# Optimization experiments

Measured on AMD Instinct MI355X. Metric: run time of the kernel, lower is better.

## Reference

```python
import jax, jax.numpy as jnp
import numpy as np

N_NODES = 100000


def gcn_conv(x, W, b, src, dst, norm, n_nodes):
    # x: [N, F_in] -> [N, F_out]; GCNConv: D^-1/2 (A+I) D^-1/2 (X W) + b
    h = x @ W                                   # [N, F_out]
    msg = h[src] * norm[:, None]                # [E+N, F_out] gather + scale
    out = jax.ops.segment_sum(msg, dst, num_segments=n_nodes)  # scatter-add
    return out + b


def setup_inputs() -> dict:
    key = jax.random.key(0)
    k0, k1, k2, k3, k4, k5 = jax.random.split(key, 6)
    n, e, f_in, f_hid, n_cls = N_NODES, 1600000, 128, 128, 3
    x = jax.random.normal(k0, (n, f_in), dtype=jnp.float32)
    edge_index = jax.random.randint(k1, (2, e), 0, n, dtype=jnp.int64)
    s1 = 1.0 / np.sqrt(f_in)
    s2 = 1.0 / np.sqrt(f_hid)
    W1 = jax.random.uniform(k2, (f_in, f_hid), jnp.float32, -s1, s1)
    b1 = jnp.zeros((f_hid,), jnp.float32)
    W2 = jax.random.uniform(k3, (f_hid, f_hid), jnp.float32, -s2, s2)
    b2 = jnp.zeros((f_hid,), jnp.float32)
    Wfc = jax.random.uniform(k4, (f_hid, n_cls), jnp.float32, -s2, s2)
    bfc = jax.random.uniform(k5, (n_cls,), jnp.float32, -s2, s2)
    return {"x": x, "edge_index": edge_index, "W1": W1, "b1": b1,
            "W2": W2, "b2": b2, "Wfc": Wfc, "bfc": bfc}


def reference(x, edge_index, W1, b1, W2, b2, Wfc, bfc):
    n = x.shape[0]
    # add self-loops (PyG GCNConv default add_self_loops=True)
    loops = jnp.arange(n, dtype=edge_index.dtype)
    src = jnp.concatenate([edge_index[0], loops])
    dst = jnp.concatenate([edge_index[1], loops])
    deg = jax.ops.segment_sum(jnp.ones_like(dst, dtype=x.dtype), dst,
                              num_segments=n)
    dinv = jax.lax.rsqrt(deg)                   # deg >= 1 due to self-loops
    norm = dinv[src] * dinv[dst]                # [E+N]
    h = jax.nn.relu(gcn_conv(x, W1, b1, src, dst, norm, n))   # dropout=eval id
    h = jax.nn.relu(gcn_conv(h, W2, b2, src, dst, norm, n))
    return jnp.tanh(h @ Wfc + bfc)              # [N, 3]
```

## Files before the change

kernel.cpp:

```cpp
#include <hip/hip_runtime.h>
#include <hip/hip_bf16.h>
#include <hip/hip_fp16.h>


#define NODE_F 128

typedef __attribute__((ext_vector_type(8))) short bf16x8;
typedef __attribute__((ext_vector_type(4))) float f32x4;

__device__ inline unsigned short bf16_rn(float x) {
    unsigned u = __builtin_bit_cast(unsigned, x);
    unsigned r = (u + 0x7fffu + ((u >> 16) & 1u)) >> 16;
    return (unsigned short)r;
}
__device__ inline float bf16_to_f(unsigned short h) {
    unsigned u = (unsigned)h << 16;
    return __builtin_bit_cast(float, u);
}


__global__ void deg_rank_kernel(const int* __restrict__ dst, int* __restrict__ degE,
                                int* __restrict__ rank, int E) {
    int i = blockIdx.x * blockDim.x + threadIdx.x;
    if (i < E) rank[i] = atomicAdd(&degE[dst[i]], 1);
}

__global__ __launch_bounds__(256) void scan_block_kernel(
    const int* __restrict__ degE, int* __restrict__ row_start,
    int* __restrict__ bsum, int N)
{
    __shared__ int s[256];
    const int tid = threadIdx.x;
    const int idx = blockIdx.x * 1024 + tid * 4;
    int v0 = (idx + 0 < N) ? degE[idx + 0] : 0;
    int v1 = (idx + 1 < N) ? degE[idx + 1] : 0;
    int v2 = (idx + 2 < N) ? degE[idx + 2] : 0;
    int v3 = (idx + 3 < N) ? degE[idx + 3] : 0;
    int t = v0 + v1 + v2 + v3;
    s[tid] = t;
    __syncthreads();
    #pragma unroll
    for (int off = 1; off < 256; off <<= 1) {
        int x = (tid >= off) ? s[tid - off] : 0;
        __syncthreads();
        s[tid] += x;
        __syncthreads();
    }
    int excl = s[tid] - t;
    if (idx + 0 < N) row_start[idx + 0] = excl;
    if (idx + 1 < N) row_start[idx + 1] = excl + v0;
    if (idx + 2 < N) row_start[idx + 2] = excl + v0 + v1;
    if (idx + 3 < N) row_start[idx + 3] = excl + v0 + v1 + v2;
    if (tid == 255) bsum[blockIdx.x] = s[255];
}

__global__ __launch_bounds__(1024) void scan_tops_kernel(int* __restrict__ bsum, int nb) {
    __shared__ int s[1024];
    const int tid = threadIdx.x;
    int v = (tid < nb) ? bsum[tid] : 0;
    s[tid] = v;
    __syncthreads();
    #pragma unroll
    for (int off = 1; off < 1024; off <<= 1) {
        int x = (tid >= off) ? s[tid - off] : 0;
        __syncthreads();
        s[tid] += x;
        __syncthreads();
    }
    if (tid < nb) bsum[tid] = s[tid] - v;
}

__global__ void scan_finish_kernel(const int* __restrict__ degE, int* __restrict__ row_start,
                                   const int* __restrict__ bsum, float* __restrict__ dinv, int N)
{
    int i = blockIdx.x * blockDim.x + threadIdx.x;
    if (i >= N) return;
    int rs = row_start[i] + bsum[i >> 10];
    row_start[i] = rs;
    dinv[i] = rsqrtf((float)degE[i] + 1.0f);
    if (i == N - 1) row_start[N] = rs + degE[i];
}


__global__ __launch_bounds__(256) void wconv_kernel(const float* __restrict__ W1,
                                                    const float* __restrict__ W2,
                                                    unsigned short* __restrict__ WhiT,
                                                    unsigned short* __restrict__ WloT)
{
    const float* W = blockIdx.x ? W2 : W1;
    unsigned short* hiT = WhiT + blockIdx.x * 128 * 128;
    unsigned short* loT = WloT + blockIdx.x * 128 * 128;
    int tid = threadIdx.x;
    for (int i = tid; i < 128 * 128; i += 256) {
        int k = i >> 7, n = i & 127;
        float x = W[i];
        unsigned short hi = bf16_rn(x);
        float lo = x - bf16_to_f(hi);
        hiT[n * 128 + k] = hi;
        loT[n * 128 + k] = bf16_rn(lo);
    }
}


template<bool RELU_IN>
__device__ __forceinline__ void gemm_body(
    const float* __restrict__ X, const unsigned short* __restrict__ WhiT,
    const unsigned short* __restrict__ WloT, const float* __restrict__ dinv,
    __half* __restrict__ Hs, int N, int bid,
    unsigned short* xhi, unsigned short* xlo)
{
    const int tid  = threadIdx.x;
    const int lane = tid & 63;
    const int w    = tid >> 6;
    const int rbase = bid * 64;

    bf16x8 bhi[2][4], blo[2][4];
    {
        int n0   = w * 32 + (lane & 15);
        int koct = (lane >> 4) * 8;
        #pragma unroll
        for (int nt = 0; nt < 2; ++nt) {
            #pragma unroll
            for (int kk = 0; kk < 4; ++kk) {
                size_t o = (size_t)(n0 + nt * 16) * 128 + kk * 32 + koct;
                bhi[nt][kk] = *reinterpret_cast<const bf16x8*>(WhiT + o);
                blo[nt][kk] = *reinterpret_cast<const bf16x8*>(WloT + o);
            }
        }
    }

    #pragma unroll
    for (int it = 0; it < 8; ++it) {
        int f   = it * 256 + tid;
        int row = f >> 5;
        int k4  = f & 31;
        float4 v = make_float4(0.f, 0.f, 0.f, 0.f);
        if (rbase + row < N)
            v = *reinterpret_cast<const float4*>(X + (size_t)(rbase + row) * NODE_F + k4 * 4);
        if (RELU_IN) {
            v.x = fmaxf(v.x, 0.f); v.y = fmaxf(v.y, 0.f);
            v.z = fmaxf(v.z, 0.f); v.w = fmaxf(v.w, 0.f);
        }
        float xs[4] = {v.x, v.y, v.z, v.w};
        ushort4 h4, l4;
        unsigned short* hp = &h4.x;
        unsigned short* lp = &l4.x;
        #pragma unroll
        for (int j = 0; j < 4; ++j) {
            unsigned short hi = bf16_rn(xs[j]);
            hp[j] = hi;
            lp[j] = bf16_rn(xs[j] - bf16_to_f(hi));
        }
        int byte = row * 256 + ((k4 * 8) ^ ((row & 7) << 4));
        *reinterpret_cast<ushort4*>(reinterpret_cast<char*>(xhi) + byte) = h4;
        *reinterpret_cast<ushort4*>(reinterpret_cast<char*>(xlo) + byte) = l4;
    }
    __syncthreads();

    f32x4 acc[4][2];
    #pragma unroll
    for (int m = 0; m < 4; ++m)
        #pragma unroll
        for (int nt = 0; nt < 2; ++nt)
            acc[m][nt] = (f32x4){0.f, 0.f, 0.f, 0.f};

    #pragma unroll
    for (int kk = 0; kk < 4; ++kk) {
        #pragma unroll
        for (int m = 0; m < 4; ++m) {
            int row  = m * 16 + (lane & 15);
            int koff = kk * 64 + (lane >> 4) * 16;
            int byte = row * 256 + (koff ^ ((row & 7) << 4));
            bf16x8 ahi = *reinterpret_cast<const bf16x8*>(reinterpret_cast<char*>(xhi) + byte);
            bf16x8 alo = *reinterpret_cast<const bf16x8*>(reinterpret_cast<char*>(xlo) + byte);
            #pragma unroll
            for (int nt = 0; nt < 2; ++nt) {
                acc[m][nt] = __builtin_amdgcn_mfma_f32_16x16x32_bf16(ahi, bhi[nt][kk], acc[m][nt], 0, 0, 0);
                acc[m][nt] = __builtin_amdgcn_mfma_f32_16x16x32_bf16(ahi, blo[nt][kk], acc[m][nt], 0, 0, 0);
                acc[m][nt] = __builtin_amdgcn_mfma_f32_16x16x32_bf16(alo, bhi[nt][kk], acc[m][nt], 0, 0, 0);
            }
        }
    }

    #pragma unroll
    for (int m = 0; m < 4; ++m) {
        int row = rbase + m * 16 + (lane >> 4) * 4;
        int col = w * 32 + (lane & 15);
        #pragma unroll
        for (int nt = 0; nt < 2; ++nt) {
            #pragma unroll
            for (int r = 0; r < 4; ++r) {
                if (row + r < N)
                    Hs[(size_t)(row + r) * NODE_F + col + nt * 16] =
                        __float2half(acc[m][nt][r] * dinv[row + r]);
            }
        }
    }
}

__global__ __launch_bounds__(256) void gemm1_fill_kernel(
    const float* __restrict__ X, const unsigned short* __restrict__ WhiT,
    const unsigned short* __restrict__ WloT, const float* __restrict__ dinv,
    __half* __restrict__ Hs, int N, int gemm_blocks,
    const int* __restrict__ src, const int* __restrict__ dst,
    const int* __restrict__ rank, const int* __restrict__ row_start,
    int* __restrict__ csr_src, int E)
{
    __shared__ unsigned short xhi[64 * 128];
    __shared__ unsigned short xlo[64 * 128];
    if (blockIdx.x < (unsigned)gemm_blocks) {
        gemm_body<false>(X, WhiT, WloT, dinv, Hs, N, blockIdx.x, xhi, xlo);
    } else {
        int e = (blockIdx.x - gemm_blocks) * 256 + threadIdx.x;
        if (e < E)
            csr_src[row_start[dst[e]] + rank[e]] = src[e];
    }
}

template<bool RELU_IN>
__global__ __launch_bounds__(256) void gemm_mfma_kernel(
    const float* __restrict__ X, const unsigned short* __restrict__ WhiT,
    const unsigned short* __restrict__ WloT, const float* __restrict__ dinv,
    __half* __restrict__ Hs, int N)
{
    __shared__ unsigned short xhi[64 * 128];
    __shared__ unsigned short xlo[64 * 128];
    gemm_body<RELU_IN>(X, WhiT, WloT, dinv, Hs, N, blockIdx.x, xhi, xlo);
}

__global__ __launch_bounds__(256) void gather_kernel(
    const __half* __restrict__ Hs, const int* __restrict__ csr_src,
    const int* __restrict__ row_start, const float* __restrict__ dinv,
    const float* __restrict__ b, float* __restrict__ acc, int N)
{
    int node = (blockIdx.x * blockDim.x + threadIdx.x) >> 6;
    int lane = threadIdx.x & 63;
    if (node >= N) return;

    const __half2* H2 = reinterpret_cast<const __half2*>(Hs);
    float2 a = __half22float2(H2[(size_t)node * 64 + lane]);

    int i   = row_start[node];
    int end = row_start[node + 1];
    for (; i + 3 < end; i += 4) {
        int s0 = csr_src[i], s1 = csr_src[i + 1], s2 = csr_src[i + 2], s3 = csr_src[i + 3];
        float2 v0 = __half22float2(H2[(size_t)s0 * 64 + lane]);
        float2 v1 = __half22float2(H2[(size_t)s1 * 64 + lane]);
        float2 v2 = __half22float2(H2[(size_t)s2 * 64 + lane]);
        float2 v3 = __half22float2(H2[(size_t)s3 * 64 + lane]);
        a.x += (v0.x + v1.x) + (v2.x + v3.x);
        a.y += (v0.y + v1.y) + (v2.y + v3.y);
    }
    for (; i < end; ++i) {
        int s = csr_src[i];
        float2 v = __half22float2(H2[(size_t)s * 64 + lane]);
        a.x += v.x;
        a.y += v.y;
    }

    const float dd = dinv[node];
    float2 bb = reinterpret_cast<const float2*>(b)[lane];
    float2 o;
    o.x = bb.x + dd * a.x;
    o.y = bb.y + dd * a.y;
    reinterpret_cast<float2*>(acc)[(size_t)node * 64 + lane] = o;
}


__global__ __launch_bounds__(256) void fc_kernel(const float* __restrict__ A,
                                                 const float* __restrict__ Wfc,
                                                 const float* __restrict__ bfc,
                                                 float* __restrict__ out, int N)
{
    int wid  = (blockIdx.x * blockDim.x + threadIdx.x) >> 6;
    int lane = threadIdx.x & 63;
    if (wid >= N) return;
    const float* row = A + (size_t)wid * NODE_F;
    float a0 = fmaxf(row[lane], 0.f);
    float a1 = fmaxf(row[lane + 64], 0.f);
    float p0 = a0 * Wfc[lane * 3 + 0] + a1 * Wfc[(lane + 64) * 3 + 0];
    float p1 = a0 * Wfc[lane * 3 + 1] + a1 * Wfc[(lane + 64) * 3 + 1];
    float p2 = a0 * Wfc[lane * 3 + 2] + a1 * Wfc[(lane + 64) * 3 + 2];
    #pragma unroll
    for (int off = 32; off > 0; off >>= 1) {
        p0 += __shfl_down(p0, off);
        p1 += __shfl_down(p1, off);
        p2 += __shfl_down(p2, off);
    }
    if (lane == 0) {
        out[(size_t)wid * 3 + 0] = tanhf(p0 + bfc[0]);
        out[(size_t)wid * 3 + 1] = tanhf(p1 + bfc[1]);
        out[(size_t)wid * 3 + 2] = tanhf(p2 + bfc[2]);
    }
}

extern "C" void kernel_launch(void* const* d_in, const int* in_sizes, int n_in,
                              void* d_out, int out_size, void* d_ws, size_t ws_size,
                              hipStream_t stream)
{
    const float* x    = (const float*)d_in[0];
    const int*   edge = (const int*)d_in[1];
    const float* W1   = (const float*)d_in[2];
    const float* b1   = (const float*)d_in[3];
    const float* W2   = (const float*)d_in[4];
    const float* b2   = (const float*)d_in[5];
    const float* Wfc  = (const float*)d_in[6];
    const float* bfc  = (const float*)d_in[7];
    float* out = (float*)d_out;

    const int N = in_sizes[0] / NODE_F;
    const int E = in_sizes[1] / 2;
    const int* src = edge;
    const int* dst = edge + E;

    char* ws = (char*)d_ws;
    size_t off = 0;
    auto alloc = [&](size_t bytes) {
        void* p = ws + off;
        off += (bytes + 511) & ~511ull;
        return p;
    };
    const int nblk1024 = (N + 1023) / 1024;
    float* dinv      = (float*)alloc((size_t)N * 4);
    int*   degE      = (int*)  alloc((size_t)N * 4);
    int*   rank      = (int*)  alloc((size_t)E * 4);
    int*   row_start = (int*)  alloc((size_t)(N + 1) * 4);
    int*   bsum      = (int*)  alloc((size_t)nblk1024 * 4);
    int*   csr_src   = (int*)  alloc((size_t)E * 4);
    unsigned short* WhiT = (unsigned short*)alloc(2 * 128 * 128 * 2);
    unsigned short* WloT = (unsigned short*)alloc(2 * 128 * 128 * 2);
    __half* Hs       = (__half*)alloc((size_t)N * NODE_F * 2);
    float*  acc      = (float*) alloc((size_t)N * NODE_F * 4);
    (void)ws_size; (void)n_in; (void)out_size;

    const int B = 256;

    wconv_kernel<<<2, B, 0, stream>>>(W1, W2, WhiT, WloT);

    hipMemsetAsync(degE, 0, (size_t)N * 4, stream);
    deg_rank_kernel<<<(E + B - 1) / B, B, 0, stream>>>(dst, degE, rank, E);
    scan_block_kernel<<<nblk1024, B, 0, stream>>>(degE, row_start, bsum, N);
    scan_tops_kernel<<<1, 1024, 0, stream>>>(bsum, nblk1024);
    scan_finish_kernel<<<(N + B - 1) / B, B, 0, stream>>>(degE, row_start, bsum, dinv, N);

    int gemm_grid   = (N + 63) / 64;
    int fill_grid   = (E + B - 1) / B;
    int gather_grid = (N + 3) / 4;

    gemm1_fill_kernel<<<gemm_grid + fill_grid, B, 0, stream>>>(
        x, WhiT, WloT, dinv, Hs, N, gemm_grid,
        src, dst, rank, row_start, csr_src, E);
    gather_kernel<<<gather_grid, B, 0, stream>>>(Hs, csr_src, row_start, dinv, b1, acc, N);

    gemm_mfma_kernel<true><<<gemm_grid, B, 0, stream>>>(acc, WhiT + 128 * 128, WloT + 128 * 128,
                                                        dinv, Hs, N);
    gather_kernel<<<gather_grid, B, 0, stream>>>(Hs, csr_src, row_start, dinv, b2, acc, N);

    fc_kernel<<<(N + 3) / 4, B, 0, stream>>>(acc, Wfc, bfc, out, N);
}
```

Baseline: 368.8 us.

## Restructure GCN pipeline: overlap GEMM1 with degree count, fuse FC into gather

GEMM1 now runs in the same launch as the degree/rank atomics and writes unscaled output. A later pass scales it by dinv alongside the CSR fill. The first gather applies ReLU and writes bf16 hi/lo splits, so the second GEMM loads pre-split inputs instead of fp32. The second gather fuses the final FC+tanh, removing the fp32 acc buffer and one launch, and both gathers unroll to 8 edges. The tradeoffs are an extra read-modify-write pass over H, with one more fp16 rounding before the dinv scale, and the hi/lo buffers written by gather1.

```diff
diff --git a/kernel.cpp b/kernel.cpp
--- a/kernel.cpp
+++ b/kernel.cpp
@@ -6,6 +6,7 @@
 #define NODE_F 128
 
 typedef __attribute__((ext_vector_type(8))) short bf16x8;
+typedef __attribute__((ext_vector_type(8))) unsigned short u16x8;
 typedef __attribute__((ext_vector_type(4))) float f32x4;
 
 __device__ inline unsigned short bf16_rn(float x) {
@@ -16,69 +17,6 @@
 __device__ inline float bf16_to_f(unsigned short h) {
     unsigned u = (unsigned)h << 16;
     return __builtin_bit_cast(float, u);
-}
-
-
-__global__ void deg_rank_kernel(const int* __restrict__ dst, int* __restrict__ degE,
-                                int* __restrict__ rank, int E) {
-    int i = blockIdx.x * blockDim.x + threadIdx.x;
-    if (i < E) rank[i] = atomicAdd(&degE[dst[i]], 1);
-}
-
-__global__ __launch_bounds__(256) void scan_block_kernel(
-    const int* __restrict__ degE, int* __restrict__ row_start,
-    int* __restrict__ bsum, int N)
-{
-    __shared__ int s[256];
-    const int tid = threadIdx.x;
-    const int idx = blockIdx.x * 1024 + tid * 4;
-    int v0 = (idx + 0 < N) ? degE[idx + 0] : 0;
-    int v1 = (idx + 1 < N) ? degE[idx + 1] : 0;
-    int v2 = (idx + 2 < N) ? degE[idx + 2] : 0;
-    int v3 = (idx + 3 < N) ? degE[idx + 3] : 0;
-    int t = v0 + v1 + v2 + v3;
-    s[tid] = t;
-    __syncthreads();
-    #pragma unroll
-    for (int off = 1; off < 256; off <<= 1) {
-        int x = (tid >= off) ? s[tid - off] : 0;
-        __syncthreads();
-        s[tid] += x;
-        __syncthreads();
-    }
-    int excl = s[tid] - t;
-    if (idx + 0 < N) row_start[idx + 0] = excl;
-    if (idx + 1 < N) row_start[idx + 1] = excl + v0;
-    if (idx + 2 < N) row_start[idx + 2] = excl + v0 + v1;
-    if (idx + 3 < N) row_start[idx + 3] = excl + v0 + v1 + v2;
-    if (tid == 255) bsum[blockIdx.x] = s[255];
-}
-
-__global__ __launch_bounds__(1024) void scan_tops_kernel(int* __restrict__ bsum, int nb) {
-    __shared__ int s[1024];
-    const int tid = threadIdx.x;
-    int v = (tid < nb) ? bsum[tid] : 0;
-    s[tid] = v;
-    __syncthreads();
-    #pragma unroll
-    for (int off = 1; off < 1024; off <<= 1) {
-        int x = (tid >= off) ? s[tid - off] : 0;
-        __syncthreads();
-        s[tid] += x;
-        __syncthreads();
-    }
-    if (tid < nb) bsum[tid] = s[tid] - v;
-}
-
-__global__ void scan_finish_kernel(const int* __restrict__ degE, int* __restrict__ row_start,
-                                   const int* __restrict__ bsum, float* __restrict__ dinv, int N)
-{
-    int i = blockIdx.x * blockDim.x + threadIdx.x;
-    if (i >= N) return;
-    int rs = row_start[i] + bsum[i >> 10];
-    row_start[i] = rs;
-    dinv[i] = rsqrtf((float)degE[i] + 1.0f);
-    if (i == N - 1) row_start[N] = rs + degE[i];
 }
 
 
@@ -102,11 +40,70 @@
 }
 
 
-template<bool RELU_IN>
+__global__ __launch_bounds__(256) void scan_block_kernel(
+    const int* __restrict__ degE, int* __restrict__ row_start,
+    int* __restrict__ bsum, int N)
+{
+    __shared__ int s[256];
+    const int tid = threadIdx.x;
+    const int idx = blockIdx.x * 1024 + tid * 4;
+    int v0 = (idx + 0 < N) ? degE[idx + 0] : 0;
+    int v1 = (idx + 1 < N) ? degE[idx + 1] : 0;
+    int v2 = (idx + 2 < N) ? degE[idx + 2] : 0;
+    int v3 = (idx + 3 < N) ? degE[idx + 3] : 0;
+    int t = v0 + v1 + v2 + v3;
+    s[tid] = t;
+    __syncthreads();
+    #pragma unroll
+    for (int off = 1; off < 256; off <<= 1) {
+        int x = (tid >= off) ? s[tid - off] : 0;
+        __syncthreads();
+        s[tid] += x;
+        __syncthreads();
+    }
+    int excl = s[tid] - t;
+    if (idx + 0 < N) row_start[idx + 0] = excl;
+    if (idx + 1 < N) row_start[idx + 1] = excl + v0;
+    if (idx + 2 < N) row_start[idx + 2] = excl + v0 + v1;
+    if (idx + 3 < N) row_start[idx + 3] = excl + v0 + v1 + v2;
+    if (tid == 255) bsum[blockIdx.x] = s[255];
+}
+
+__global__ __launch_bounds__(1024) void scan_tops_kernel(int* __restrict__ bsum, int nb) {
+    __shared__ int s[1024];
+    const int tid = threadIdx.x;
+    int v = (tid < nb) ? bsum[tid] : 0;
+    s[tid] = v;
+    __syncthreads();
+    #pragma unroll
+    for (int off = 1; off < 1024; off <<= 1) {
+        int x = (tid >= off) ? s[tid - off] : 0;
+        __syncthreads();
+        s[tid] += x;
+        __syncthreads();
+    }
+    if (tid < nb) bsum[tid] = s[tid] - v;
+}
+
+__global__ void scan_finish_kernel(const int* __restrict__ degE, int* __restrict__ row_start,
+                                   const int* __restrict__ bsum, float* __restrict__ dinv, int N)
+{
+    int i = blockIdx.x * blockDim.x + threadIdx.x;
+    if (i >= N) return;
+    int rs = row_start[i] + bsum[i >> 10];
+    row_start[i] = rs;
+    dinv[i] = rsqrtf((float)degE[i] + 1.0f);
+    if (i == N - 1) row_start[N] = rs + degE[i];
+}
+
+
+template<bool SPLIT_IN, bool SCALE_OUT>
 __device__ __forceinline__ void gemm_body(
-    const float* __restrict__ X, const unsigned short* __restrict__ WhiT,
-    const unsigned short* __restrict__ WloT, const float* __restrict__ dinv,
-    __half* __restrict__ Hs, int N, int bid,
+    const float* __restrict__ Xf,
+    const unsigned short* __restrict__ Xhi_g, const unsigned short* __restrict__ Xlo_g,
+    const unsigned short* __restrict__ WhiT, const unsigned short* __restrict__ WloT,
+    const float* __restrict__ dinv,
+    __half* __restrict__ Hout, int N, int bid,
     unsigned short* xhi, unsigned short* xlo)
 {
     const int tid  = threadIdx.x;
@@ -129,31 +126,46 @@
         }
     }
 
-    #pragma unroll
-    for (int it = 0; it < 8; ++it) {
-        int f   = it * 256 + tid;
-        int row = f >> 5;
-        int k4  = f & 31;
-        float4 v = make_float4(0.f, 0.f, 0.f, 0.f);
-        if (rbase + row < N)
-            v = *reinterpret_cast<const float4*>(X + (size_t)(rbase + row) * NODE_F + k4 * 4);
-        if (RELU_IN) {
-            v.x = fmaxf(v.x, 0.f); v.y = fmaxf(v.y, 0.f);
-            v.z = fmaxf(v.z, 0.f); v.w = fmaxf(v.w, 0.f);
-        }
-        float xs[4] = {v.x, v.y, v.z, v.w};
-        ushort4 h4, l4;
-        unsigned short* hp = &h4.x;
-        unsigned short* lp = &l4.x;
-        #pragma unroll
-        for (int j = 0; j < 4; ++j) {
-            unsigned short hi = bf16_rn(xs[j]);
-            hp[j] = hi;
-            lp[j] = bf16_rn(xs[j] - bf16_to_f(hi));
-        }
-        int byte = row * 256 + ((k4 * 8) ^ ((row & 7) << 4));
-        *reinterpret_cast<ushort4*>(reinterpret_cast<char*>(xhi) + byte) = h4;
-        *reinterpret_cast<ushort4*>(reinterpret_cast<char*>(xlo) + byte) = l4;
+    if (!SPLIT_IN) {
+        #pragma unroll
+        for (int it = 0; it < 8; ++it) {
+            int f   = it * 256 + tid;
+            int row = f >> 5;
+            int k4  = f & 31;
+            float4 v = make_float4(0.f, 0.f, 0.f, 0.f);
+            if (rbase + row < N)
+                v = *reinterpret_cast<const float4*>(Xf + (size_t)(rbase + row) * NODE_F + k4 * 4);
+            float xs[4] = {v.x, v.y, v.z, v.w};
+            ushort4 h4, l4;
+            unsigned short* hp = &h4.x;
+            unsigned short* lp = &l4.x;
+            #pragma unroll
+            for (int j = 0; j < 4; ++j) {
+                unsigned short hi = bf16_rn(xs[j]);
+                hp[j] = hi;
+                lp[j] = bf16_rn(xs[j] - bf16_to_f(hi));
+            }
+            int byte = row * 256 + ((k4 * 8) ^ ((row & 7) << 4));
+            *reinterpret_cast<ushort4*>(reinterpret_cast<char*>(xhi) + byte) = h4;
+            *reinterpret_cast<ushort4*>(reinterpret_cast<char*>(xlo) + byte) = l4;
+        }
+    } else {
+        #pragma unroll
+        for (int it = 0; it < 4; ++it) {
+            int idx = it * 256 + tid;
+            int row = idx >> 4;
+            int k8  = idx & 15;
+            u16x8 h = {0, 0, 0, 0, 0, 0, 0, 0};
+            u16x8 l = {0, 0, 0, 0, 0, 0, 0, 0};
+            if (rbase + row < N) {
+                size_t g = (size_t)(rbase + row) * NODE_F + k8 * 8;
+                h = *reinterpret_cast<const u16x8*>(Xhi_g + g);
+                l = *reinterpret_cast<const u16x8*>(Xlo_g + g);
+            }
+            int byte = row * 256 + ((k8 * 16) ^ ((row & 7) << 4));
+            *reinterpret_cast<u16x8*>(reinterpret_cast<char*>(xhi) + byte) = h;
+            *reinterpret_cast<u16x8*>(reinterpret_cast<char*>(xlo) + byte) = l;
+        }
     }
     __syncthreads();
 
@@ -190,48 +202,66 @@
         for (int nt = 0; nt < 2; ++nt) {
             #pragma unroll
             for (int r = 0; r < 4; ++r) {
-                if (row + r < N)
-                    Hs[(size_t)(row + r) * NODE_F + col + nt * 16] =
-                        __float2half(acc[m][nt][r] * dinv[row + r]);
-            }
-        }
-    }
-}
-
-__global__ __launch_bounds__(256) void gemm1_fill_kernel(
+                if (row + r < N) {
+                    float v = acc[m][nt][r];
+                    if (SCALE_OUT) v *= dinv[row + r];
+                    Hout[(size_t)(row + r) * NODE_F + col + nt * 16] = __float2half(v);
+                }
+            }
+        }
+    }
+}
+
+
+__global__ __launch_bounds__(256) void hybridA_kernel(
+    const int* __restrict__ dst, int* __restrict__ degE, int* __restrict__ rank,
+    int E, int deg_blocks,
     const float* __restrict__ X, const unsigned short* __restrict__ WhiT,
-    const unsigned short* __restrict__ WloT, const float* __restrict__ dinv,
-    __half* __restrict__ Hs, int N, int gemm_blocks,
+    const unsigned short* __restrict__ WloT, __half* __restrict__ H, int N)
+{
+    __shared__ unsigned short xhi[64 * 128];
+    __shared__ unsigned short xlo[64 * 128];
+    if ((int)blockIdx.x < deg_blocks) {
+        int e = blockIdx.x * 256 + threadIdx.x;
+        if (e < E) rank[e] = atomicAdd(&degE[dst[e]], 1);
+    } else {
+        gemm_body<false, false>(X, nullptr, nullptr, WhiT, WloT, nullptr,
+                                H, N, blockIdx.x - deg_blocks, xhi, xlo);
+    }
+}
+
+
+__global__ __launch_bounds__(256) void hybridB_kernel(
     const int* __restrict__ src, const int* __restrict__ dst,
     const int* __restrict__ rank, const int* __restrict__ row_start,
-    int* __restrict__ csr_src, int E)
-{
-    __shared__ unsigned short xhi[64 * 128];
-    __shared__ unsigned short xlo[64 * 128];
-    if (blockIdx.x < (unsigned)gemm_blocks) {
-        gemm_body<false>(X, WhiT, WloT, dinv, Hs, N, blockIdx.x, xhi, xlo);
+    int* __restrict__ csr_src, int E, int fill_blocks,
+    __half* __restrict__ H, const int* __restrict__ degE, int N)
+{
+    if ((int)blockIdx.x < fill_blocks) {
+        int e = blockIdx.x * 256 + threadIdx.x;
+        if (e < E) csr_src[row_start[dst[e]] + rank[e]] = src[e];
     } else {
-        int e = (blockIdx.x - gemm_blocks) * 256 + threadIdx.x;
-        if (e < E)
-            csr_src[row_start[dst[e]] + rank[e]] = src[e];
-    }
-}
-
-template<bool RELU_IN>
-__global__ __launch_bounds__(256) void gemm_mfma_kernel(
-    const float* __restrict__ X, const unsigned short* __restrict__ WhiT,
-    const unsigned short* __restrict__ WloT, const float* __restrict__ dinv,
-    __half* __restrict__ Hs, int N)
-{
-    __shared__ unsigned short xhi[64 * 128];
-    __shared__ unsigned short xlo[64 * 128];
-    gemm_body<RELU_IN>(X, WhiT, WloT, dinv, Hs, N, blockIdx.x, xhi, xlo);
-}
-
-__global__ __launch_bounds__(256) void gather_kernel(
+        int idx = (blockIdx.x - fill_blocks) * 256 + threadIdx.x;
+        if (idx < N * 16) {
+            int row = idx >> 4;
+            float ds = rsqrtf((float)degE[row] + 1.0f);
+            __half2* p = reinterpret_cast<__half2*>(H) + (size_t)idx * 4;
+            #pragma unroll
+            for (int j = 0; j < 4; ++j) {
+                float2 v = __half22float2(p[j]);
+                v.x *= ds; v.y *= ds;
+                p[j] = __float22half2_rn(v);
+            }
+        }
+    }
+}
+
+
+__global__ __launch_bounds__(256) void gather1_kernel(
     const __half* __restrict__ Hs, const int* __restrict__ csr_src,
     const int* __restrict__ row_start, const float* __restrict__ dinv,
-    const float* __restrict__ b, float* __restrict__ acc, int N)
+    const float* __restrict__ b,
+    unsigned short* __restrict__ Xhi, unsigned short* __restrict__ Xlo, int N)
 {
     int node = (blockIdx.x * blockDim.x + threadIdx.x) >> 6;
     int lane = threadIdx.x & 63;
@@ -242,14 +272,19 @@
 
     int i   = row_start[node];
     int end = row_start[node + 1];
-    for (; i + 3 < end; i += 4) {
-        int s0 = csr_src[i], s1 = csr_src[i + 1], s2 = csr_src[i + 2], s3 = csr_src[i + 3];
+    for (; i + 7 < end; i += 8) {
+        int s0 = csr_src[i + 0], s1 = csr_src[i + 1], s2 = csr_src[i + 2], s3 = csr_src[i + 3];
+        int s4 = csr_src[i + 4], s5 = csr_src[i + 5], s6 = csr_src[i + 6], s7 = csr_src[i + 7];
         float2 v0 = __half22float2(H2[(size_t)s0 * 64 + lane]);
         float2 v1 = __half22float2(H2[(size_t)s1 * 64 + lane]);
         float2 v2 = __half22float2(H2[(size_t)s2 * 64 + lane]);
         float2 v3 = __half22float2(H2[(size_t)s3 * 64 + lane]);
-        a.x += (v0.x + v1.x) + (v2.x + v3.x);
-        a.y += (v0.y + v1.y) + (v2.y + v3.y);
+        float2 v4 = __half22float2(H2[(size_t)s4 * 64 + lane]);
+        float2 v5 = __half22float2(H2[(size_t)s5 * 64 + lane]);
+        float2 v6 = __half22float2(H2[(size_t)s6 * 64 + lane]);
+        float2 v7 = __half22float2(H2[(size_t)s7 * 64 + lane]);
+        a.x += ((v0.x + v1.x) + (v2.x + v3.x)) + ((v4.x + v5.x) + (v6.x + v7.x));
+        a.y += ((v0.y + v1.y) + (v2.y + v3.y)) + ((v4.y + v5.y) + (v6.y + v7.y));
     }
     for (; i < end; ++i) {
         int s = csr_src[i];
@@ -260,27 +295,61 @@
 
     const float dd = dinv[node];
     float2 bb = reinterpret_cast<const float2*>(b)[lane];
-    float2 o;
-    o.x = bb.x + dd * a.x;
-    o.y = bb.y + dd * a.y;
-    reinterpret_cast<float2*>(acc)[(size_t)node * 64 + lane] = o;
-}
-
-
-__global__ __launch_bounds__(256) void fc_kernel(const float* __restrict__ A,
-                                                 const float* __restrict__ Wfc,
-                                                 const float* __restrict__ bfc,
-                                                 float* __restrict__ out, int N)
-{
-    int wid  = (blockIdx.x * blockDim.x + threadIdx.x) >> 6;
+    float rx = fmaxf(bb.x + dd * a.x, 0.f);
+    float ry = fmaxf(bb.y + dd * a.y, 0.f);
+    unsigned short hx = bf16_rn(rx), hy = bf16_rn(ry);
+    unsigned short lx = bf16_rn(rx - bf16_to_f(hx));
+    unsigned short ly = bf16_rn(ry - bf16_to_f(hy));
+    reinterpret_cast<ushort2*>(Xhi)[(size_t)node * 64 + lane] = make_ushort2(hx, hy);
+    reinterpret_cast<ushort2*>(Xlo)[(size_t)node * 64 + lane] = make_ushort2(lx, ly);
+}
+
+
+__global__ __launch_bounds__(256) void gather2fc_kernel(
+    const __half* __restrict__ Hs, const int* __restrict__ csr_src,
+    const int* __restrict__ row_start, const float* __restrict__ dinv,
+    const float* __restrict__ b, const float* __restrict__ Wfc,
+    const float* __restrict__ bfc, float* __restrict__ out, int N)
+{
+    int node = (blockIdx.x * blockDim.x + threadIdx.x) >> 6;
     int lane = threadIdx.x & 63;
-    if (wid >= N) return;
-    const float* row = A + (size_t)wid * NODE_F;
-    float a0 = fmaxf(row[lane], 0.f);
-    float a1 = fmaxf(row[lane + 64], 0.f);
-    float p0 = a0 * Wfc[lane * 3 + 0] + a1 * Wfc[(lane + 64) * 3 + 0];
-    float p1 = a0 * Wfc[lane * 3 + 1] + a1 * Wfc[(lane + 64) * 3 + 1];
-    float p2 = a0 * Wfc[lane * 3 + 2] + a1 * Wfc[(lane + 64) * 3 + 2];
+    if (node >= N) return;
+
+    const __half2* H2 = reinterpret_cast<const __half2*>(Hs);
+    float2 a = __half22float2(H2[(size_t)node * 64 + lane]);
+
+    int i   = row_start[node];
+    int end = row_start[node + 1];
+    for (; i + 7 < end; i += 8) {
+        int s0 = csr_src[i + 0], s1 = csr_src[i + 1], s2 = csr_src[i + 2], s3 = csr_src[i + 3];
+        int s4 = csr_src[i + 4], s5 = csr_src[i + 5], s6 = csr_src[i + 6], s7 = csr_src[i + 7];
+        float2 v0 = __half22float2(H2[(size_t)s0 * 64 + lane]);
+        float2 v1 = __half22float2(H2[(size_t)s1 * 64 + lane]);
+        float2 v2 = __half22float2(H2[(size_t)s2 * 64 + lane]);
+        float2 v3 = __half22float2(H2[(size_t)s3 * 64 + lane]);
+        float2 v4 = __half22float2(H2[(size_t)s4 * 64 + lane]);
+        float2 v5 = __half22float2(H2[(size_t)s5 * 64 + lane]);
+        float2 v6 = __half22float2(H2[(size_t)s6 * 64 + lane]);
+        float2 v7 = __half22float2(H2[(size_t)s7 * 64 + lane]);
+        a.x += ((v0.x + v1.x) + (v2.x + v3.x)) + ((v4.x + v5.x) + (v6.x + v7.x));
+        a.y += ((v0.y + v1.y) + (v2.y + v3.y)) + ((v4.y + v5.y) + (v6.y + v7.y));
+    }
+    for (; i < end; ++i) {
+        int s = csr_src[i];
+        float2 v = __half22float2(H2[(size_t)s * 64 + lane]);
+        a.x += v.x;
+        a.y += v.y;
+    }
+
+    const float dd = dinv[node];
+    float2 bb = reinterpret_cast<const float2*>(b)[lane];
+    float rx = fmaxf(bb.x + dd * a.x, 0.f);
+    float ry = fmaxf(bb.y + dd * a.y, 0.f);
+
+    const float* w0 = Wfc + (size_t)(2 * lane) * 3;
+    float p0 = rx * w0[0] + ry * w0[3];
+    float p1 = rx * w0[1] + ry * w0[4];
+    float p2 = rx * w0[2] + ry * w0[5];
     #pragma unroll
     for (int off = 32; off > 0; off >>= 1) {
         p0 += __shfl_down(p0, off);
@@ -288,10 +357,22 @@
         p2 += __shfl_down(p2, off);
     }
     if (lane == 0) {
-        out[(size_t)wid * 3 + 0] = tanhf(p0 + bfc[0]);
-        out[(size_t)wid * 3 + 1] = tanhf(p1 + bfc[1]);
-        out[(size_t)wid * 3 + 2] = tanhf(p2 + bfc[2]);
-    }
+        out[(size_t)node * 3 + 0] = tanhf(p0 + bfc[0]);
+        out[(size_t)node * 3 + 1] = tanhf(p1 + bfc[1]);
+        out[(size_t)node * 3 + 2] = tanhf(p2 + bfc[2]);
+    }
+}
+
+
+__global__ __launch_bounds__(256) void gemm2_kernel(
+    const unsigned short* __restrict__ Xhi_g, const unsigned short* __restrict__ Xlo_g,
+    const unsigned short* __restrict__ WhiT, const unsigned short* __restrict__ WloT,
+    const float* __restrict__ dinv, __half* __restrict__ Hs, int N)
+{
+    __shared__ unsigned short xhi[64 * 128];
+    __shared__ unsigned short xlo[64 * 128];
+    gemm_body<true, true>(nullptr, Xhi_g, Xlo_g, WhiT, WloT, dinv,
+                          Hs, N, blockIdx.x, xhi, xlo);
 }
 
 extern "C" void kernel_launch(void* const* d_in, const int* in_sizes, int n_in,
@@ -330,31 +411,34 @@
     unsigned short* WhiT = (unsigned short*)alloc(2 * 128 * 128 * 2);
     unsigned short* WloT = (unsigned short*)alloc(2 * 128 * 128 * 2);
     __half* Hs       = (__half*)alloc((size_t)N * NODE_F * 2);
-    float*  acc      = (float*) alloc((size_t)N * NODE_F * 4);
+    unsigned short* Xhi = (unsigned short*)alloc((size_t)N * NODE_F * 2);
+    unsigned short* Xlo = (unsigned short*)alloc((size_t)N * NODE_F * 2);
     (void)ws_size; (void)n_in; (void)out_size;
 
     const int B = 256;
+    const int gemm_grid   = (N + 63) / 64;
+    const int edge_grid   = (E + B - 1) / B;
+    const int scale_grid  = (N * 16 + B - 1) / B;
+    const int gather_grid = (N + 3) / 4;
 
     wconv_kernel<<<2, B, 0, stream>>>(W1, W2, WhiT, WloT);
-
     hipMemsetAsync(degE, 0, (size_t)N * 4, stream);
-    deg_rank_kernel<<<(E + B - 1) / B, B, 0, stream>>>(dst, degE, rank, E);
+
+    hybridA_kernel<<<edge_grid + gemm_grid, B, 0, stream>>>(
+        dst, degE, rank, E, edge_grid, x, WhiT, WloT, Hs, N);
+
     scan_block_kernel<<<nblk1024, B, 0, stream>>>(degE, row_start, bsum, N);
     scan_tops_kernel<<<1, 1024, 0, stream>>>(bsum, nblk1024);
     scan_finish_kernel<<<(N + B - 1) / B, B, 0, stream>>>(degE, row_start, bsum, dinv, N);
 
-    int gemm_grid   = (N + 63) / 64;
-    int fill_grid   = (E + B - 1) / B;
-    int gather_grid = (N + 3) / 4;
-
-    gemm1_fill_kernel<<<gemm_grid + fill_grid, B, 0, stream>>>(
-        x, WhiT, WloT, dinv, Hs, N, gemm_grid,
-        src, dst, rank, row_start, csr_src, E);
-    gather_kernel<<<gather_grid, B, 0, stream>>>(Hs, csr_src, row_start, dinv, b1, acc, N);
-
-    gemm_mfma_kernel<true><<<gemm_grid, B, 0, stream>>>(acc, WhiT + 128 * 128, WloT + 128 * 128,
-                                                        dinv, Hs, N);
-    gather_kernel<<<gather_grid, B, 0, stream>>>(Hs, csr_src, row_start, dinv, b2, acc, N);
-
-    fc_kernel<<<(N + 3) / 4, B, 0, stream>>>(acc, Wfc, bfc, out, N);
-}
+    hybridB_kernel<<<edge_grid + scale_grid, B, 0, stream>>>(
+        src, dst, rank, row_start, csr_src, E, edge_grid, Hs, degE, N);
+
+    gather1_kernel<<<gather_grid, B, 0, stream>>>(Hs, csr_src, row_start, dinv, b1, Xhi, Xlo, N);
+
+    gemm2_kernel<<<gemm_grid, B, 0, stream>>>(Xhi, Xlo, WhiT + 128 * 128, WloT + 128 * 128,
+                                              dinv, Hs, N);
+
+    gather2fc_kernel<<<gather_grid, B, 0, stream>>>(Hs, csr_src, row_start, dinv, b2,
+                                                    Wfc, bfc, out, N);
+}
```

Result: faster. 352.0 us (-4.6%).
